# Kernel optimization log

Measured on AMD Instinct MI355X. Metric: run time of the kernel, lower is better.

The kernel has to match this reference:

```python
import jax, jax.numpy as jnp
import numpy as np

NUM_GROUPS = 32
EPS = 1e-5


def setup_inputs() -> dict:
    key = jax.random.key(0)
    k1, k2 = jax.random.split(key)
    N, C = 1000000, 128
    num_instances = 100
    features = jax.random.normal(k1, (N, C), dtype=jnp.float32)
    ins_indices_batch = jax.random.randint(k2, (N,), 0, num_instances, dtype=jnp.int64)
    gamma = jnp.ones((C,), dtype=jnp.float32)
    beta = jnp.zeros((C,), dtype=jnp.float32)
    return {
        "features": features,
        "ins_indices_batch": ins_indices_batch,
        "gamma": gamma,
        "beta": beta,
        "num_instances": num_instances,
    }


def reference(features, ins_indices_batch, gamma, beta, num_instances):
    # Segmented GroupNorm: for each instance id i, the original gathers rows
    # where ins_indices_batch == i into a [1, C, L] tensor and applies
    # nn.GroupNorm(G, C): stats over (C//G channels x L positions) per group.
    N, C = features.shape
    G = NUM_GROUPS
    Cg = C // G
    seg = ins_indices_batch.astype(jnp.int32)

    # Per-(segment, channel) sums -> per-(segment, group) stats. Single pass.
    sums = jax.ops.segment_sum(features, seg, num_segments=num_instances)        # [S, C]
    sqs = jax.ops.segment_sum(features * features, seg, num_segments=num_instances)  # [S, C]
    cnt = jax.ops.segment_sum(jnp.ones((N,), features.dtype), seg, num_segments=num_instances)  # [S]

    gsum = sums.reshape(num_instances, G, Cg).sum(axis=-1)   # [S, G]
    gsq = sqs.reshape(num_instances, G, Cg).sum(axis=-1)     # [S, G]
    denom = jnp.maximum(cnt[:, None] * Cg, 1.0)               # [S, G]
    mean = gsum / denom
    var = gsq / denom - mean * mean                            # biased var (GroupNorm)
    inv = jax.lax.rsqrt(var + EPS)                             # [S, G]

    # Scatter stats back to each row and normalize (fused elementwise).
    mean_n = mean[seg]  # [N, G]
    inv_n = inv[seg]    # [N, G]
    xg = features.reshape(N, G, Cg)
    xn = (xg - mean_n[:, :, None]) * inv_n[:, :, None]
    out = xn.reshape(N, C) * gamma + beta
    return out
```

## Files before the change

### kernel.cpp

```cpp
#include <hip/hip_runtime.h>
#include <hip/hip_bf16.h>


#define C_CHANNELS 128
#define GROUPS 32
#define SEG_CAP 256
#define LDS_SEG_CAP 128
#define EPS 1e-5f

__global__ __launch_bounds__(256) void gn_pass1(
    const float4* __restrict__ x, const int* __restrict__ seg,
    float* __restrict__ gsum, float* __restrict__ gsq, float* __restrict__ gcnt,
    const int* __restrict__ nInstPtr, int N)
{
    __shared__ float lsum[LDS_SEG_CAP * GROUPS];
    __shared__ float lsq [LDS_SEG_CAP * GROUPS];
    __shared__ float lcnt[LDS_SEG_CAP];

    for (int i = threadIdx.x; i < LDS_SEG_CAP * GROUPS; i += blockDim.x) {
        lsum[i] = 0.f; lsq[i] = 0.f;
    }
    for (int i = threadIdx.x; i < LDS_SEG_CAP; i += blockDim.x) lcnt[i] = 0.f;
    __syncthreads();

    const int g = threadIdx.x & 31;
    const long long total  = (long long)N * GROUPS;
    const long long stride = (long long)gridDim.x * blockDim.x;
    long long i = (long long)blockIdx.x * blockDim.x + threadIdx.x;

    for (; i + stride < total; i += 2 * stride) {
        long long i2 = i + stride;
        int row1 = (int)(i  >> 5);
        int row2 = (int)(i2 >> 5);
        float4 v1 = x[i];
        float4 v2 = x[i2];
        int s1 = seg[row1];
        int s2 = seg[row2];
        float sum1 = (v1.x + v1.y) + (v1.z + v1.w);
        float sq1  = v1.x*v1.x + v1.y*v1.y + v1.z*v1.z + v1.w*v1.w;
        float sum2 = (v2.x + v2.y) + (v2.z + v2.w);
        float sq2  = v2.x*v2.x + v2.y*v2.y + v2.z*v2.z + v2.w*v2.w;
        if (s1 < LDS_SEG_CAP) {
            atomicAdd(&lsum[s1*GROUPS + g], sum1);
            atomicAdd(&lsq [s1*GROUPS + g], sq1);
            if (g == 0) atomicAdd(&lcnt[s1], 1.0f);
        } else {
            atomicAdd(&gsum[s1*GROUPS + g], sum1);
            atomicAdd(&gsq [s1*GROUPS + g], sq1);
            if (g == 0) atomicAdd(&gcnt[s1], 1.0f);
        }
        if (s2 < LDS_SEG_CAP) {
            atomicAdd(&lsum[s2*GROUPS + g], sum2);
            atomicAdd(&lsq [s2*GROUPS + g], sq2);
            if (g == 0) atomicAdd(&lcnt[s2], 1.0f);
        } else {
            atomicAdd(&gsum[s2*GROUPS + g], sum2);
            atomicAdd(&gsq [s2*GROUPS + g], sq2);
            if (g == 0) atomicAdd(&gcnt[s2], 1.0f);
        }
    }
    for (; i < total; i += stride) {
        int row = (int)(i >> 5);
        float4 v = x[i];
        int s = seg[row];
        float sum = (v.x + v.y) + (v.z + v.w);
        float sq  = v.x*v.x + v.y*v.y + v.z*v.z + v.w*v.w;
        if (s < LDS_SEG_CAP) {
            atomicAdd(&lsum[s*GROUPS + g], sum);
            atomicAdd(&lsq [s*GROUPS + g], sq);
            if (g == 0) atomicAdd(&lcnt[s], 1.0f);
        } else {
            atomicAdd(&gsum[s*GROUPS + g], sum);
            atomicAdd(&gsq [s*GROUPS + g], sq);
            if (g == 0) atomicAdd(&gcnt[s], 1.0f);
        }
    }
    __syncthreads();

    int S = *nInstPtr;
    int lim = min(S, LDS_SEG_CAP);
    int nb = lim * GROUPS;
    int rot = (int)((blockIdx.x * 64u) % (unsigned)nb);
    for (int t = threadIdx.x; t < nb; t += blockDim.x) {
        int j = t + rot; if (j >= nb) j -= nb;
        float a = lsum[j], b = lsq[j];
        if (a != 0.f || b != 0.f) {
            atomicAdd(&gsum[j], a);
            atomicAdd(&gsq [j], b);
        }
    }
    for (int t = threadIdx.x; t < lim; t += blockDim.x) {
        float c = lcnt[t];
        if (c != 0.f) atomicAdd(&gcnt[t], c);
    }
}

__global__ __launch_bounds__(256) void gn_finalize(
    const float* __restrict__ gsum, const float* __restrict__ gsq,
    const float* __restrict__ gcnt, float2* __restrict__ stats,
    const int* __restrict__ nInstPtr)
{
    int S = *nInstPtr;
    int i = blockIdx.x * blockDim.x + threadIdx.x;
    if (i < S * GROUPS) {
        int s = i >> 5;
        float cnt = gcnt[s];
        float denom = fmaxf(cnt * 4.0f, 1.0f);
        float mean = gsum[i] / denom;
        float var  = gsq[i] / denom - mean * mean;
        float inv  = rsqrtf(var + EPS);
        stats[i] = make_float2(mean, inv);
    }
}

__global__ __launch_bounds__(256) void gn_pass2(
    const float4* __restrict__ x, const int* __restrict__ seg,
    const float2* __restrict__ stats,
    const float4* __restrict__ gamma4, const float4* __restrict__ beta4,
    float4* __restrict__ out, int N)
{
    const int g = threadIdx.x & 31;
    const float4 gm = gamma4[g];
    const float4 bt = beta4[g];
    const long long total  = (long long)N * GROUPS;
    const long long stride = (long long)gridDim.x * blockDim.x;
    for (long long i = (long long)blockIdx.x * blockDim.x + threadIdx.x;
         i < total; i += stride) {
        int row = (int)(i >> 5);
        float4 v = x[i];
        int s = seg[row];
        float2 mi = stats[s * GROUPS + g];
        float4 o;
        o.x = (v.x - mi.x) * mi.y * gm.x + bt.x;
        o.y = (v.y - mi.x) * mi.y * gm.y + bt.y;
        o.z = (v.z - mi.x) * mi.y * gm.z + bt.z;
        o.w = (v.w - mi.x) * mi.y * gm.w + bt.w;
        out[i] = o;
    }
}

extern "C" void kernel_launch(void* const* d_in, const int* in_sizes, int n_in,
                              void* d_out, int out_size, void* d_ws, size_t ws_size,
                              hipStream_t stream) {
    const float* feat  = (const float*)d_in[0];
    const int*   seg   = (const int*)d_in[1];
    const float* gamma = (const float*)d_in[2];
    const float* beta  = (const float*)d_in[3];
    const int*   nInst = (const int*)d_in[4];
    const int N = in_sizes[0] / C_CHANNELS;

    float* gsum = (float*)d_ws;
    float* gsq  = gsum + SEG_CAP * GROUPS;
    float* gcnt = gsq  + SEG_CAP * GROUPS;
    float2* stats = (float2*)(gcnt + SEG_CAP);
    size_t zero_bytes = (size_t)(2 * SEG_CAP * GROUPS + SEG_CAP) * sizeof(float);

    hipMemsetAsync(d_ws, 0, zero_bytes, stream);

    gn_pass1<<<512, 256, 0, stream>>>(
        (const float4*)feat, seg, gsum, gsq, gcnt, nInst, N);

    gn_finalize<<<(SEG_CAP * GROUPS + 255) / 256, 256, 0, stream>>>(
        gsum, gsq, gcnt, stats, nInst);

    gn_pass2<<<2048, 256, 0, stream>>>(
        (const float4*)feat, seg, stats,
        (const float4*)gamma, (const float4*)beta,
        (float4*)d_out, N);
}
```

Baseline: 1.108 ms.

## Tune both passes: raw LDS atomics, 4x unroll, LDS stats cache, nontemporal stores

```diff
diff --git a/kernel.cpp b/kernel.cpp
--- a/kernel.cpp
+++ b/kernel.cpp
@@ -1,12 +1,23 @@
 #include <hip/hip_runtime.h>
-#include <hip/hip_bf16.h>
 
 
 #define C_CHANNELS 128
 #define GROUPS 32
 #define SEG_CAP 256
-#define LDS_SEG_CAP 128
+#define LDS_SEG_CAP 104
 #define EPS 1e-5f
+
+typedef float f32x4 __attribute__((ext_vector_type(4)));
+
+__device__ __forceinline__ void lds_fadd(float* p, float v) {
+    asm volatile("ds_add_f32 %0, %1"
+                 :: "v"((unsigned)(unsigned long long)p), "v"(v));
+}
+
+__device__ __forceinline__ void nt_store4(float4* p, const float4& v) {
+    f32x4 t; t.x = v.x; t.y = v.y; t.z = v.z; t.w = v.w;
+    __builtin_nontemporal_store(t, (f32x4*)p);
+}
 
 __global__ __launch_bounds__(256) void gn_pass1(
     const float4* __restrict__ x, const int* __restrict__ seg,
@@ -17,64 +28,93 @@
     __shared__ float lsq [LDS_SEG_CAP * GROUPS];
     __shared__ float lcnt[LDS_SEG_CAP];
 
-    for (int i = threadIdx.x; i < LDS_SEG_CAP * GROUPS; i += blockDim.x) {
-        lsum[i] = 0.f; lsq[i] = 0.f;
-    }
-    for (int i = threadIdx.x; i < LDS_SEG_CAP; i += blockDim.x) lcnt[i] = 0.f;
+    for (int t = threadIdx.x; t < LDS_SEG_CAP * GROUPS; t += blockDim.x) {
+        lsum[t] = 0.f; lsq[t] = 0.f;
+    }
+    for (int t = threadIdx.x; t < LDS_SEG_CAP; t += blockDim.x) lcnt[t] = 0.f;
     __syncthreads();
 
     const int g = threadIdx.x & 31;
     const long long total  = (long long)N * GROUPS;
     const long long stride = (long long)gridDim.x * blockDim.x;
+    const int rowStride = (int)(stride >> 5);
     long long i = (long long)blockIdx.x * blockDim.x + threadIdx.x;
 
-    for (; i + stride < total; i += 2 * stride) {
-        long long i2 = i + stride;
-        int row1 = (int)(i  >> 5);
-        int row2 = (int)(i2 >> 5);
-        float4 v1 = x[i];
-        float4 v2 = x[i2];
-        int s1 = seg[row1];
-        int s2 = seg[row2];
-        float sum1 = (v1.x + v1.y) + (v1.z + v1.w);
-        float sq1  = v1.x*v1.x + v1.y*v1.y + v1.z*v1.z + v1.w*v1.w;
-        float sum2 = (v2.x + v2.y) + (v2.z + v2.w);
-        float sq2  = v2.x*v2.x + v2.y*v2.y + v2.z*v2.z + v2.w*v2.w;
+    for (; i + 3 * stride < total; i += 4 * stride) {
+        int row0 = (int)(i >> 5);
+        float4 v0 = x[i];
+        float4 v1 = x[i + stride];
+        float4 v2 = x[i + 2 * stride];
+        float4 v3 = x[i + 3 * stride];
+        int s0 = seg[row0];
+        int s1 = seg[row0 + rowStride];
+        int s2 = seg[row0 + 2 * rowStride];
+        int s3 = seg[row0 + 3 * rowStride];
+
+        float a0 = (v0.x + v0.y) + (v0.z + v0.w);
+        float q0 = v0.x*v0.x + v0.y*v0.y + v0.z*v0.z + v0.w*v0.w;
+        float a1 = (v1.x + v1.y) + (v1.z + v1.w);
+        float q1 = v1.x*v1.x + v1.y*v1.y + v1.z*v1.z + v1.w*v1.w;
+        float a2 = (v2.x + v2.y) + (v2.z + v2.w);
+        float q2 = v2.x*v2.x + v2.y*v2.y + v2.z*v2.z + v2.w*v2.w;
+        float a3 = (v3.x + v3.y) + (v3.z + v3.w);
+        float q3 = v3.x*v3.x + v3.y*v3.y + v3.z*v3.z + v3.w*v3.w;
+
+        if (s0 < LDS_SEG_CAP) {
+            lds_fadd(&lsum[s0 * GROUPS + g], a0);
+            lds_fadd(&lsq [s0 * GROUPS + g], q0);
+            if (g == 0) lds_fadd(&lcnt[s0], 1.0f);
+        } else {
+            unsafeAtomicAdd(&gsum[s0 * GROUPS + g], a0);
+            unsafeAtomicAdd(&gsq [s0 * GROUPS + g], q0);
+            if (g == 0) unsafeAtomicAdd(&gcnt[s0], 1.0f);
+        }
         if (s1 < LDS_SEG_CAP) {
-            atomicAdd(&lsum[s1*GROUPS + g], sum1);
-            atomicAdd(&lsq [s1*GROUPS + g], sq1);
-            if (g == 0) atomicAdd(&lcnt[s1], 1.0f);
-        } else {
-            atomicAdd(&gsum[s1*GROUPS + g], sum1);
-            atomicAdd(&gsq [s1*GROUPS + g], sq1);
-            if (g == 0) atomicAdd(&gcnt[s1], 1.0f);
+            lds_fadd(&lsum[s1 * GROUPS + g], a1);
+            lds_fadd(&lsq [s1 * GROUPS + g], q1);
+            if (g == 0) lds_fadd(&lcnt[s1], 1.0f);
+        } else {
+            unsafeAtomicAdd(&gsum[s1 * GROUPS + g], a1);
+            unsafeAtomicAdd(&gsq [s1 * GROUPS + g], q1);
+            if (g == 0) unsafeAtomicAdd(&gcnt[s1], 1.0f);
         }
         if (s2 < LDS_SEG_CAP) {
-            atomicAdd(&lsum[s2*GROUPS + g], sum2);
-            atomicAdd(&lsq [s2*GROUPS + g], sq2);
-            if (g == 0) atomicAdd(&lcnt[s2], 1.0f);
-        } else {
-            atomicAdd(&gsum[s2*GROUPS + g], sum2);
-            atomicAdd(&gsq [s2*GROUPS + g], sq2);
-            if (g == 0) atomicAdd(&gcnt[s2], 1.0f);
+            lds_fadd(&lsum[s2 * GROUPS + g], a2);
+            lds_fadd(&lsq [s2 * GROUPS + g], q2);
+            if (g == 0) lds_fadd(&lcnt[s2], 1.0f);
+        } else {
+            unsafeAtomicAdd(&gsum[s2 * GROUPS + g], a2);
+            unsafeAtomicAdd(&gsq [s2 * GROUPS + g], q2);
+            if (g == 0) unsafeAtomicAdd(&gcnt[s2], 1.0f);
+        }
+        if (s3 < LDS_SEG_CAP) {
+            lds_fadd(&lsum[s3 * GROUPS + g], a3);
+            lds_fadd(&lsq [s3 * GROUPS + g], q3);
+            if (g == 0) lds_fadd(&lcnt[s3], 1.0f);
+        } else {
+            unsafeAtomicAdd(&gsum[s3 * GROUPS + g], a3);
+            unsafeAtomicAdd(&gsq [s3 * GROUPS + g], q3);
+            if (g == 0) unsafeAtomicAdd(&gcnt[s3], 1.0f);
         }
     }
     for (; i < total; i += stride) {
         int row = (int)(i >> 5);
         float4 v = x[i];
         int s = seg[row];
-        float sum = (v.x + v.y) + (v.z + v.w);
-        float sq  = v.x*v.x + v.y*v.y + v.z*v.z + v.w*v.w;
+        float a = (v.x + v.y) + (v.z + v.w);
+        float q = v.x*v.x + v.y*v.y + v.z*v.z + v.w*v.w;
         if (s < LDS_SEG_CAP) {
-            atomicAdd(&lsum[s*GROUPS + g], sum);
-            atomicAdd(&lsq [s*GROUPS + g], sq);
-            if (g == 0) atomicAdd(&lcnt[s], 1.0f);
-        } else {
-            atomicAdd(&gsum[s*GROUPS + g], sum);
-            atomicAdd(&gsq [s*GROUPS + g], sq);
-            if (g == 0) atomicAdd(&gcnt[s], 1.0f);
-        }
-    }
+            lds_fadd(&lsum[s * GROUPS + g], a);
+            lds_fadd(&lsq [s * GROUPS + g], q);
+            if (g == 0) lds_fadd(&lcnt[s], 1.0f);
+        } else {
+            unsafeAtomicAdd(&gsum[s * GROUPS + g], a);
+            unsafeAtomicAdd(&gsq [s * GROUPS + g], q);
+            if (g == 0) unsafeAtomicAdd(&gcnt[s], 1.0f);
+        }
+    }
+
+    asm volatile("s_waitcnt lgkmcnt(0)" ::: "memory");
     __syncthreads();
 
     int S = *nInstPtr;
@@ -85,13 +125,13 @@
         int j = t + rot; if (j >= nb) j -= nb;
         float a = lsum[j], b = lsq[j];
         if (a != 0.f || b != 0.f) {
-            atomicAdd(&gsum[j], a);
-            atomicAdd(&gsq [j], b);
+            unsafeAtomicAdd(&gsum[j], a);
+            unsafeAtomicAdd(&gsq [j], b);
         }
     }
     for (int t = threadIdx.x; t < lim; t += blockDim.x) {
         float c = lcnt[t];
-        if (c != 0.f) atomicAdd(&gcnt[t], c);
+        if (c != 0.f) unsafeAtomicAdd(&gcnt[t], c);
     }
 }
 
@@ -117,25 +157,65 @@
     const float4* __restrict__ x, const int* __restrict__ seg,
     const float2* __restrict__ stats,
     const float4* __restrict__ gamma4, const float4* __restrict__ beta4,
-    float4* __restrict__ out, int N)
+    float4* __restrict__ out, const int* __restrict__ nInstPtr, int N)
 {
+    __shared__ float lmean[LDS_SEG_CAP * GROUPS];
+    __shared__ float linv [LDS_SEG_CAP * GROUPS];
+    int S = *nInstPtr;
+    int lim = min(S, LDS_SEG_CAP) * GROUPS;
+    for (int t = threadIdx.x; t < lim; t += blockDim.x) {
+        float2 mi = stats[t];
+        lmean[t] = mi.x; linv[t] = mi.y;
+    }
+    __syncthreads();
+
     const int g = threadIdx.x & 31;
     const float4 gm = gamma4[g];
     const float4 bt = beta4[g];
     const long long total  = (long long)N * GROUPS;
     const long long stride = (long long)gridDim.x * blockDim.x;
-    for (long long i = (long long)blockIdx.x * blockDim.x + threadIdx.x;
-         i < total; i += stride) {
+    const int rowStride = (int)(stride >> 5);
+    long long i = (long long)blockIdx.x * blockDim.x + threadIdx.x;
+
+    for (; i + stride < total; i += 2 * stride) {
+        int row0 = (int)(i >> 5);
+        float4 v0 = x[i];
+        float4 v1 = x[i + stride];
+        int s0 = seg[row0];
+        int s1 = seg[row0 + rowStride];
+
+        float m0, iv0, m1, iv1;
+        if (s0 < LDS_SEG_CAP) { m0 = lmean[s0 * GROUPS + g]; iv0 = linv[s0 * GROUPS + g]; }
+        else { float2 t = stats[s0 * GROUPS + g]; m0 = t.x; iv0 = t.y; }
+        if (s1 < LDS_SEG_CAP) { m1 = lmean[s1 * GROUPS + g]; iv1 = linv[s1 * GROUPS + g]; }
+        else { float2 t = stats[s1 * GROUPS + g]; m1 = t.x; iv1 = t.y; }
+
+        float4 o0, o1;
+        o0.x = (v0.x - m0) * iv0 * gm.x + bt.x;
+        o0.y = (v0.y - m0) * iv0 * gm.y + bt.y;
+        o0.z = (v0.z - m0) * iv0 * gm.z + bt.z;
+        o0.w = (v0.w - m0) * iv0 * gm.w + bt.w;
+        o1.x = (v1.x - m1) * iv1 * gm.x + bt.x;
+        o1.y = (v1.y - m1) * iv1 * gm.y + bt.y;
+        o1.z = (v1.z - m1) * iv1 * gm.z + bt.z;
+        o1.w = (v1.w - m1) * iv1 * gm.w + bt.w;
+
+        nt_store4(&out[i], o0);
+        nt_store4(&out[i + stride], o1);
+    }
+    for (; i < total; i += stride) {
         int row = (int)(i >> 5);
         float4 v = x[i];
         int s = seg[row];
-        float2 mi = stats[s * GROUPS + g];
+        float m, iv;
+        if (s < LDS_SEG_CAP) { m = lmean[s * GROUPS + g]; iv = linv[s * GROUPS + g]; }
+        else { float2 t = stats[s * GROUPS + g]; m = t.x; iv = t.y; }
         float4 o;
-        o.x = (v.x - mi.x) * mi.y * gm.x + bt.x;
-        o.y = (v.y - mi.x) * mi.y * gm.y + bt.y;
-        o.z = (v.z - mi.x) * mi.y * gm.z + bt.z;
-        o.w = (v.w - mi.x) * mi.y * gm.w + bt.w;
-        out[i] = o;
+        o.x = (v.x - m) * iv * gm.x + bt.x;
+        o.y = (v.y - m) * iv * gm.y + bt.y;
+        o.z = (v.z - m) * iv * gm.z + bt.z;
+        o.w = (v.w - m) * iv * gm.w + bt.w;
+        nt_store4(&out[i], o);
     }
 }
 
@@ -155,16 +235,16 @@
     float2* stats = (float2*)(gcnt + SEG_CAP);
     size_t zero_bytes = (size_t)(2 * SEG_CAP * GROUPS + SEG_CAP) * sizeof(float);
 
-    hipMemsetAsync(d_ws, 0, zero_bytes, stream);
-
-    gn_pass1<<<512, 256, 0, stream>>>(
+    (void)hipMemsetAsync(d_ws, 0, zero_bytes, stream);
+
+    gn_pass1<<<1536, 256, 0, stream>>>(
         (const float4*)feat, seg, gsum, gsq, gcnt, nInst, N);
 
     gn_finalize<<<(SEG_CAP * GROUPS + 255) / 256, 256, 0, stream>>>(
         gsum, gsq, gcnt, stats, nInst);
 
-    gn_pass2<<<2048, 256, 0, stream>>>(
+    gn_pass2<<<1536, 256, 0, stream>>>(
         (const float4*)feat, seg, stats,
         (const float4*)gamma, (const float4*)beta,
-        (float4*)d_out, N);
-}
+        (float4*)d_out, nInst, N);
+}
```

Result: no change. 1.119 ms (+1.0%).
